# Performance work log

Hardware: AMD Instinct MI355X
Metric: run time of the kernel (lower is better)

Reference implementation:

```python
import jax, jax.numpy as jnp
import numpy as np

B, M, N = 128, 512, 512
THRESH = 0.5  # parsed from stop_strategy 'threshold_0.5'
AVG_DEG = 16.0


def setup_inputs() -> dict:
    key = jax.random.key(0)
    k1, k2, k3 = jax.random.split(key, 3)
    y_pred = jax.random.uniform(k1, (B, M, N), dtype=jnp.float32)

    def make_adj(k, n):
        a = (jax.random.uniform(k, (B, n, n)) < (AVG_DEG / n)).astype(jnp.float32)
        a = jnp.maximum(a, jnp.swapaxes(a, 1, 2))          # symmetric
        return a * (1.0 - jnp.eye(n, dtype=jnp.float32))   # no self loops

    return {"y_pred": y_pred, "adj1": make_adj(k2, M), "adj2": make_adj(k3, N)}


def _frontier(adj, v):
    # neighbors of selected nodes that are not yet selected
    return jnp.minimum(adj @ v, 1.0) * (1.0 - v)


def _search_one(y, a1, a2):
    """Greedy MCS tree search for one graph pair. y: (M,N), a1: (M,M), a2: (N,N)."""
    m, n = y.shape

    def cond(s):
        return s[0]

    def body(s):
        cont, v1, v2, tree, fmask = s
        masked = y * fmask
        mx = jnp.max(masked)
        new_cont = mx >= THRESH                 # stop check BEFORE commit (original order)
        idx = jnp.argmax(masked)
        i, j = idx // n, idx % n
        v1n = v1.at[i].set(1.0)
        v2n = v2.at[j].set(1.0)
        treen = tree.at[i, j].set(1.0)
        fmn = _frontier(a1, v1n)[:, None] * _frontier(a2, v2n)[None, :]
        pick = lambda new, old: jnp.where(new_cont, new, old)
        return (new_cont, pick(v1n, v1), pick(v2n, v2), pick(treen, tree), pick(fmn, fmask))

    init = (jnp.array(True),
            jnp.zeros((m,), jnp.float32),
            jnp.zeros((n,), jnp.float32),
            jnp.zeros((m, n), jnp.float32),
            jnp.ones((m, n), jnp.float32))
    final = jax.lax.while_loop(cond, body, init)
    return final[3]  # tree_pred match matrix


@jax.jit
def _search_batch(y_pred, adj1, adj2):
    return jax.vmap(_search_one)(y_pred, adj1, adj2)


def reference(y_pred, adj1, adj2):
    # returns the tree_pred match matrices for every pair in the batch
    return _search_batch(y_pred, adj1, adj2)
```

## Files before the change

kernel.cpp:

```cpp
#include <hip/hip_runtime.h>
#include <stdint.h>

#define MDIM 512
#define NDIM 512
#define NTHREADS 512

typedef unsigned long long u64;

__device__ __forceinline__ u64 wave_max_u64(u64 v) {
#pragma unroll
  for (int off = 32; off; off >>= 1) {
    u64 q = __shfl_xor(v, off);
    if (q > v) v = q;
  }
  return v;
}

__global__ __launch_bounds__(NTHREADS, 1) void tree_search_kernel(
    const float* __restrict__ y,
    const float* __restrict__ a1,
    const float* __restrict__ a2,
    float* __restrict__ out)
{
  const int b   = blockIdx.x;
  const int tid = threadIdx.x;
  const float* __restrict__ Y  = y  + (size_t)b * (MDIM * NDIM);
  const float* __restrict__ A1 = a1 + (size_t)b * (MDIM * MDIM);
  const float* __restrict__ A2 = a2 + (size_t)b * (NDIM * NDIM);
  float* __restrict__ O = out + (size_t)b * (MDIM * NDIM);

  __shared__ unsigned rowState[MDIM];
  __shared__ float    rowMax[MDIM];
  __shared__ unsigned rowArg[MDIM];
  __shared__ unsigned colState[NDIM];
  __shared__ unsigned colList[NDIM];
  __shared__ unsigned colPos[NDIM];
  __shared__ unsigned newCols[NDIM];
  __shared__ unsigned addRows[MDIM];
  __shared__ int s_colCount, s_nAdd, s_nNew, s_stop, s_ci, s_cj;
  __shared__ u64 s_part[NTHREADS / 64];

  rowState[tid] = 0u;
  colState[tid] = 0u;
  rowMax[tid]   = 0.f;
  rowArg[tid]   = 511u;
  if (tid == 0) { s_colCount = 0; s_nAdd = 0; s_nNew = 0; s_stop = 0; }
  __syncthreads();

  {
    u64 best = 0;
    for (int base = tid * 4; base < MDIM * NDIM; base += NTHREADS * 4) {
      const float4 v = *reinterpret_cast<const float4*>(Y + base);
      const float vv[4] = {v.x, v.y, v.z, v.w};
#pragma unroll
      for (int c = 0; c < 4; ++c) {
        u64 p = ((u64)__float_as_uint(vv[c]) << 32)
                | (u64)(262143u - (unsigned)(base + c));
        if (p > best) best = p;
      }
    }
    best = wave_max_u64(best);
    if ((tid & 63) == 0) s_part[tid >> 6] = best;
    __syncthreads();
    if (tid == 0) {
      u64 bst = s_part[0];
#pragma unroll
      for (int w = 1; w < NTHREADS / 64; ++w) if (s_part[w] > bst) bst = s_part[w];
      float v = __uint_as_float((unsigned)(bst >> 32));
      if (v >= 0.5f) {
        unsigned key = 262143u - (unsigned)(bst & 0xFFFFFFFFu);
        int bi = key >> 9, bj = key & 511;
        rowState[bi] = 3u;
        colState[bj] = 2u;
        O[key] = 1.0f;
        s_ci = bi; s_cj = bj;
      } else {
        s_stop = 1;
      }
    }
    __syncthreads();
  }

  while (!s_stop) {
    {
      const int r = tid;
      const unsigned st = rowState[r];
      const float av = A1[(size_t)s_ci * MDIM + r];
      const bool newRow   = (av != 0.f) && (st == 0u);
      const bool recompute = (st == 1u) && (rowArg[r] == (unsigned)s_cj);
      if (newRow || recompute) {
        rowState[r] = 2u;
        addRows[atomicAdd(&s_nAdd, 1)] = (unsigned)r;
      }
      const float bv = A2[(size_t)s_cj * NDIM + r];
      if (bv != 0.f && colState[r] == 0u) {
        colState[r] = 1u;
        newCols[atomicAdd(&s_nNew, 1)] = (unsigned)r;
        int p = atomicAdd(&s_colCount, 1);
        colList[p] = (unsigned)r;
        colPos[r]  = (unsigned)p;
      }
    }
    __syncthreads();

    {
      const int r = tid;
      if (rowState[r] == 1u) {
        float rm = rowMax[r];
        unsigned ra = rowArg[r];
        const int nn = s_nNew;
        for (int k = 0; k < nn; ++k) {
          const unsigned c = newCols[k];
          const float v = Y[((unsigned)r << 9) + c];
          if (v > rm || (v == rm && c < ra)) { rm = v; ra = c; }
        }
        rowMax[r] = rm; rowArg[r] = ra;
      }
    }
    __syncthreads();

    {
      const int g = tid >> 3, lane = tid & 7;
      const int nAdd = s_nAdd, cc = s_colCount;
      for (int a = g; a < nAdd; a += NTHREADS / 8) {
        const int rr = (int)addRows[a];
        float rm = 0.f;
        unsigned ra = 511u;
        for (int k = lane; k < cc; k += 8) {
          const unsigned c = colList[k];
          const float v = Y[((unsigned)rr << 9) + c];
          if (v > rm || (v == rm && c < ra)) { rm = v; ra = c; }
        }
        u64 p = ((u64)__float_as_uint(rm) << 32) | (u64)(511u - ra);
#pragma unroll
        for (int off = 4; off; off >>= 1) {
          u64 q = __shfl_xor(p, off, 8);
          if (q > p) p = q;
        }
        if (lane == 0) {
          rowMax[rr]   = __uint_as_float((unsigned)(p >> 32));
          rowArg[rr]   = 511u - (unsigned)(p & 0xFFFFFFFFu);
          rowState[rr] = 1u;
        }
      }
    }
    __syncthreads();

    {
      u64 cand = 0;
      if (rowState[tid] == 1u) {
        const unsigned key = ((unsigned)tid << 9) | rowArg[tid];
        cand = ((u64)__float_as_uint(rowMax[tid]) << 32)
               | (u64)(262143u - key);
      }
      cand = wave_max_u64(cand);
      if ((tid & 63) == 0) s_part[tid >> 6] = cand;
    }
    __syncthreads();

    if (tid == 0) {
      u64 bst = s_part[0];
#pragma unroll
      for (int w = 1; w < NTHREADS / 64; ++w) if (s_part[w] > bst) bst = s_part[w];
      const float v = __uint_as_float((unsigned)(bst >> 32));
      if (v >= 0.5f) {
        const unsigned key = 262143u - (unsigned)(bst & 0xFFFFFFFFu);
        const int bi = key >> 9, bj = key & 511;
        rowState[bi] = 3u;
        colState[bj] = 2u;
        const int p    = (int)colPos[bj];
        const int last = (int)colList[s_colCount - 1];
        colList[p]    = (unsigned)last;
        colPos[last]  = (unsigned)p;
        s_colCount--;
        O[key] = 1.0f;
        s_ci = bi; s_cj = bj;
        s_nAdd = 0; s_nNew = 0;
      } else {
        s_stop = 1;
      }
    }
    __syncthreads();
  }
}

extern "C" void kernel_launch(void* const* d_in, const int* in_sizes, int n_in,
                              void* d_out, int out_size, void* d_ws, size_t ws_size,
                              hipStream_t stream) {
  const float* y  = (const float*)d_in[0];
  const float* a1 = (const float*)d_in[1];
  const float* a2 = (const float*)d_in[2];
  float* out = (float*)d_out;
  const int B = in_sizes[0] / (MDIM * NDIM);

  (void)hipMemsetAsync(d_out, 0, (size_t)out_size * sizeof(float), stream);
  tree_search_kernel<<<B, NTHREADS, 0, stream>>>(y, a1, a2, out);
}
```

Before: 3.664 ms.

## Transpose score matrix into workspace for coalesced per-row incremental column updates

Adds a tiled transpose kernel that writes Y^T into the workspace, so the per-row incremental max update over newly added columns reads YT[c][r], which is contiguous across threads. The update loop now runs on all threads with an activity predicate, so the loads stay uniform. This replaces strided scattered gathers with coalesced ones, at the cost of an extra full pass over the batch of Y (read plus write) and the need for workspace. If the workspace is too small, it falls back to the old path.

```diff
diff --git a/kernel.cpp b/kernel.cpp
--- a/kernel.cpp
+++ b/kernel.cpp
@@ -16,8 +16,29 @@
   return v;
 }
 
+__global__ __launch_bounds__(256) void transpose_kernel(
+    const float* __restrict__ in, float* __restrict__ out)
+{
+  __shared__ float tile[32][33];
+  const int b = blockIdx.z;
+  const float* __restrict__ I = in  + (size_t)b * (MDIM * NDIM);
+  float* __restrict__ O       = out + (size_t)b * (MDIM * NDIM);
+  const int x  = blockIdx.x * 32 + threadIdx.x;
+  const int y0 = blockIdx.y * 32 + threadIdx.y;
+#pragma unroll
+  for (int dy = 0; dy < 32; dy += 8)
+    tile[threadIdx.y + dy][threadIdx.x] = I[(size_t)(y0 + dy) * NDIM + x];
+  __syncthreads();
+  const int xo = blockIdx.y * 32 + threadIdx.x;
+  const int yo = blockIdx.x * 32 + threadIdx.y;
+#pragma unroll
+  for (int dy = 0; dy < 32; dy += 8)
+    O[(size_t)(yo + dy) * MDIM + xo] = tile[threadIdx.x][threadIdx.y + dy];
+}
+
 __global__ __launch_bounds__(NTHREADS, 1) void tree_search_kernel(
     const float* __restrict__ y,
+    const float* __restrict__ yt,
     const float* __restrict__ a1,
     const float* __restrict__ a2,
     float* __restrict__ out)
@@ -25,6 +46,7 @@
   const int b   = blockIdx.x;
   const int tid = threadIdx.x;
   const float* __restrict__ Y  = y  + (size_t)b * (MDIM * NDIM);
+  const float* __restrict__ YT = yt ? yt + (size_t)b * (MDIM * NDIM) : nullptr;
   const float* __restrict__ A1 = a1 + (size_t)b * (MDIM * MDIM);
   const float* __restrict__ A2 = a2 + (size_t)b * (NDIM * NDIM);
   float* __restrict__ O = out + (size_t)b * (MDIM * NDIM);
@@ -105,17 +127,24 @@
 
     {
       const int r = tid;
-      if (rowState[r] == 1u) {
-        float rm = rowMax[r];
-        unsigned ra = rowArg[r];
-        const int nn = s_nNew;
+      const bool active = (rowState[r] == 1u);
+      float rm = rowMax[r];
+      unsigned ra = rowArg[r];
+      const int nn = s_nNew;
+      if (YT) {
+        for (int k = 0; k < nn; ++k) {
+          const unsigned c = newCols[k];
+          const float v = YT[((unsigned)c << 9) + (unsigned)r];
+          if (active && (v > rm || (v == rm && c < ra))) { rm = v; ra = c; }
+        }
+      } else {
         for (int k = 0; k < nn; ++k) {
           const unsigned c = newCols[k];
           const float v = Y[((unsigned)r << 9) + c];
-          if (v > rm || (v == rm && c < ra)) { rm = v; ra = c; }
-        }
-        rowMax[r] = rm; rowArg[r] = ra;
-      }
+          if (active && (v > rm || (v == rm && c < ra))) { rm = v; ra = c; }
+        }
+      }
+      if (active) { rowMax[r] = rm; rowArg[r] = ra; }
     }
     __syncthreads();
 
@@ -194,5 +223,13 @@
   const int B = in_sizes[0] / (MDIM * NDIM);
 
   (void)hipMemsetAsync(d_out, 0, (size_t)out_size * sizeof(float), stream);
-  tree_search_kernel<<<B, NTHREADS, 0, stream>>>(y, a1, a2, out);
-}
+
+  const size_t yt_bytes = (size_t)B * MDIM * NDIM * sizeof(float);
+  float* yt = nullptr;
+  if (ws_size >= yt_bytes) {
+    yt = (float*)d_ws;
+    dim3 tb(32, 8, 1), tg(NDIM / 32, MDIM / 32, B);
+    transpose_kernel<<<tg, tb, 0, stream>>>(y, yt);
+  }
+  tree_search_kernel<<<B, NTHREADS, 0, stream>>>(y, yt, a1, a2, out);
+}
```

New measurement: 3.701 ms. About the same (+1.0%).
